# Performance work log

Hardware: AMD Instinct MI355X
Metric: run time of the kernel (lower is better)

Reference implementation:

```python
import jax, jax.numpy as jnp
import numpy as np

N = 8192   # instances in bag
L = 384    # feature dim (dino_bloom_small -> self.L = 384)
D = 128    # attention hidden dim (self.D)
C = 5      # class_count


def setup_inputs() -> dict:
    key = jax.random.key(0)
    ks = jax.random.split(key, 9)
    s = 0.05
    return {
        "x": jax.random.normal(ks[0], (N, L), dtype=jnp.float32),
        # attention_multi_column: Linear(L,D) -> Tanh -> Linear(D,C)
        "aW1": jax.random.normal(ks[1], (L, D), dtype=jnp.float32) * s,
        "ab1": jax.random.normal(ks[2], (D,), dtype=jnp.float32) * s,
        "aW2": jax.random.normal(ks[3], (D, C), dtype=jnp.float32) * s,
        "ab2": jax.random.normal(ks[4], (C,), dtype=jnp.float32) * s,
        # per-class classifiers: Linear(L,64) -> ReLU -> Linear(64,1), batched over C
        "cW1": jax.random.normal(ks[5], (C, L, 64), dtype=jnp.float32) * s,
        "cb1": jax.random.normal(ks[6], (C, 64), dtype=jnp.float32) * s,
        "cW2": jax.random.normal(ks[7], (C, 64), dtype=jnp.float32) * s,
        "cb2": jax.random.normal(ks[8], (C,), dtype=jnp.float32) * s,
    }


def _pairwise_euclidean(ft):
    # ||a-b|| via Gram expansion; avoids the O(N^2*L) broadcast intermediate
    sq = jnp.sum(ft * ft, axis=1)                      # [N]
    d2 = sq[:, None] + sq[None, :] - 2.0 * (ft @ ft.T)  # [N,N]
    d2 = jnp.maximum(d2, 0.0)
    # safe sqrt (zero on diagonal, matches torch.norm subgradient convention)
    return jnp.where(d2 > 0.0, jnp.sqrt(jnp.where(d2 > 0.0, d2, 1.0)), 0.0)


def reference(x, aW1, ab1, aW2, ab2, cW1, cb1, cW2, cb2):
    ft = x  # encoder is identity for dino_bloom_small
    dist = _pairwise_euclidean(ft)                      # [N,N]
    # multicolumn attention: logits per class, softmax over instances
    att = jnp.tanh(ft @ aW1 + ab1) @ aW2 + ab2          # [N,C]
    att_sm = jax.nn.softmax(att, axis=0)                # softmax over N per class
    bag = att_sm.T @ ft                                 # [C,L] bag features per class
    # per-class classifier heads, batched over class dim
    h = jax.nn.relu(jnp.einsum('cl,clh->ch', bag, cW1) + cb1)  # [C,64]
    pred = jnp.sum(h * cW2, axis=1) + cb2               # [C]
    return pred[None, :], dist
```

## Files before the change

kernel.cpp:

```cpp
#include <hip/hip_runtime.h>
#include <cstdint>
#include <cstddef>

#define N_INST 8192
#define L_DIM  384
#define D_DIM  128
#define C_CLS  5

typedef __bf16 bf16x8 __attribute__((ext_vector_type(8)));
typedef float  f32x4  __attribute__((ext_vector_type(4)));
typedef float  f32x4u __attribute__((ext_vector_type(4), aligned(4)));

typedef __attribute__((address_space(1))) void gvoid_t;
typedef __attribute__((address_space(3))) void lvoid_t;

__device__ __forceinline__ unsigned short f2bf(float f) {
  unsigned u = __float_as_uint(f);
  unsigned r = (u + 0x7FFFu + ((u >> 16) & 1u)) >> 16;
  return (unsigned short)r;
}
__device__ __forceinline__ float bf2f(unsigned short b) {
  return __uint_as_float(((unsigned)b) << 16);
}

__device__ __forceinline__ void gload_lds16(const void* g, void* lds) {
  __builtin_amdgcn_global_load_lds(
      (gvoid_t*)(uintptr_t)g,
      (lvoid_t*)(uint32_t)(uintptr_t)lds,
      16, 0, 0);
}

__global__ __launch_bounds__(256) void prep_x_kernel(
    const float* __restrict__ x, unsigned short* __restrict__ xbf,
    float* __restrict__ sq) {
  int w = threadIdx.x >> 6, lane = threadIdx.x & 63;
  int row = blockIdx.x * 4 + w;
  const float* xr = x + (size_t)row * L_DIM;
  unsigned short* br = xbf + (size_t)row * L_DIM;
  float s = 0.f;
#pragma unroll
  for (int k = 0; k < 6; ++k) {
    float v = xr[lane + 64 * k];
    unsigned short b = f2bf(v);
    br[lane + 64 * k] = b;
    float vb = bf2f(b);
    s = fmaf(vb, vb, s);
  }
#pragma unroll
  for (int off = 32; off; off >>= 1) s += __shfl_down(s, off, 64);
  if (lane == 0) sq[row] = s;
}

__global__ __launch_bounds__(256) void prep_w_kernel(
    const float* __restrict__ aW1, unsigned short* __restrict__ w1t) {
  int idx = blockIdx.x * 256 + threadIdx.x;
  int d = idx / L_DIM, l = idx - d * L_DIM;
  w1t[idx] = f2bf(aW1[(size_t)l * D_DIM + d]);
}

__global__ __launch_bounds__(256, 2) void attn_gemm_kernel(
    const unsigned short* __restrict__ amat,
    const unsigned short* __restrict__ bmat,
    const float* __restrict__ bias,
    float* __restrict__ out) {
  __shared__ alignas(16) unsigned short As[128][64];
  __shared__ alignas(16) unsigned short Bs[128][64];

  int tid = threadIdx.x;
  int w = tid >> 6, lane = tid & 63;
  int wr = w >> 1, wc = w & 1;
  int i0 = blockIdx.x * 128;

  const unsigned short* asrc = amat + (size_t)i0 * L_DIM;
  const unsigned short* bsrc = bmat;

  f32x4 acc[4][4];
#pragma unroll
  for (int m = 0; m < 4; ++m)
#pragma unroll
    for (int n = 0; n < 4; ++n) acc[m][n] = (f32x4){0.f, 0.f, 0.f, 0.f};

  int lrow = lane & 15, lkb = lane >> 4;

  for (int kc = 0; kc < 6; ++kc) {
    int k0 = kc * 64;
#pragma unroll
    for (int c = 0; c < 4; ++c) {
      int rb = c * 32 + w * 8;
      gload_lds16(asrc + (size_t)(rb + (lane >> 3)) * L_DIM + k0 + (lane & 7) * 8,
                  &As[rb][0]);
      gload_lds16(bsrc + (size_t)(rb + (lane >> 3)) * L_DIM + k0 + (lane & 7) * 8,
                  &Bs[rb][0]);
    }
    __syncthreads();
#pragma unroll
    for (int kk = 0; kk < 64; kk += 32) {
      bf16x8 af[4], bfr[4];
#pragma unroll
      for (int m = 0; m < 4; ++m)
        af[m] = *(const bf16x8*)&As[wr * 64 + m * 16 + lrow][kk + lkb * 8];
#pragma unroll
      for (int n = 0; n < 4; ++n)
        bfr[n] = *(const bf16x8*)&Bs[wc * 64 + n * 16 + lrow][kk + lkb * 8];
#pragma unroll
      for (int m = 0; m < 4; ++m)
#pragma unroll
        for (int n = 0; n < 4; ++n)
          acc[m][n] = __builtin_amdgcn_mfma_f32_16x16x32_bf16(
              bfr[n], af[m], acc[m][n], 0, 0, 0);
    }
    __syncthreads();
  }
#pragma unroll
  for (int m = 0; m < 4; ++m) {
    int gi = i0 + wr * 64 + m * 16 + lrow;
    float* orow = out + (size_t)gi * D_DIM;
#pragma unroll
    for (int n = 0; n < 4; ++n) {
      int d0 = wc * 64 + n * 16 + lkb * 4;
      f32x4 bv = *(const f32x4*)&bias[d0];
      f32x4 o;
#pragma unroll
      for (int r = 0; r < 4; ++r) o[r] = tanhf(acc[m][n][r] + bv[r]);
      *(f32x4*)&orow[d0] = o;
    }
  }
}

__global__ __launch_bounds__(256, 2) void dist_kernel(
    const unsigned short* __restrict__ xbf, const float* __restrict__ sqv,
    float* __restrict__ F) {
  __shared__ alignas(16) unsigned short As[128][64];
  __shared__ alignas(16) unsigned short Bs[128][64];

  int tid = threadIdx.x;
  int w = tid >> 6, lane = tid & 63;
  int wr = w >> 1, wc = w & 1;

  int b = blockIdx.x;
  int bs = (b & 7) * 512 + (b >> 3);
  int ti = bs >> 6, tj = bs & 63;
  int i0 = ti * 128, j0 = tj * 128;

  const unsigned short* asrc = xbf + (size_t)i0 * L_DIM;
  const unsigned short* bsrc = xbf + (size_t)j0 * L_DIM;

  f32x4 acc[4][4];
#pragma unroll
  for (int m = 0; m < 4; ++m)
#pragma unroll
    for (int n = 0; n < 4; ++n) acc[m][n] = (f32x4){0.f, 0.f, 0.f, 0.f};

  int lrow = lane & 15, lkb = lane >> 4;

  for (int kc = 0; kc < 6; ++kc) {
    int k0 = kc * 64;
#pragma unroll
    for (int c = 0; c < 4; ++c) {
      int rb = c * 32 + w * 8;
      gload_lds16(asrc + (size_t)(rb + (lane >> 3)) * L_DIM + k0 + (lane & 7) * 8,
                  &As[rb][0]);
      gload_lds16(bsrc + (size_t)(rb + (lane >> 3)) * L_DIM + k0 + (lane & 7) * 8,
                  &Bs[rb][0]);
    }
    __syncthreads();
#pragma unroll
    for (int kk = 0; kk < 64; kk += 32) {
      bf16x8 af[4], bfr[4];
#pragma unroll
      for (int m = 0; m < 4; ++m)
        af[m] = *(const bf16x8*)&As[wr * 64 + m * 16 + lrow][kk + lkb * 8];
#pragma unroll
      for (int n = 0; n < 4; ++n)
        bfr[n] = *(const bf16x8*)&Bs[wc * 64 + n * 16 + lrow][kk + lkb * 8];
#pragma unroll
      for (int m = 0; m < 4; ++m)
#pragma unroll
        for (int n = 0; n < 4; ++n)
          acc[m][n] = __builtin_amdgcn_mfma_f32_16x16x32_bf16(
              bfr[n], af[m], acc[m][n], 0, 0, 0);
    }
    __syncthreads();
  }

#pragma unroll
  for (int m = 0; m < 4; ++m) {
    int gi = i0 + wr * 64 + m * 16 + lrow;
    float si = sqv[gi];
    float* orow = F + 5 + (size_t)gi * N_INST;
#pragma unroll
    for (int n = 0; n < 4; ++n) {
      int gjb = j0 + wc * 64 + n * 16 + lkb * 4;
      f32x4 sj = *(const f32x4*)&sqv[gjb];
      f32x4u o;
#pragma unroll
      for (int r = 0; r < 4; ++r) {
        float d2 = si + sj[r] - 2.f * acc[m][n][r];
        float dv = (d2 > 0.f) ? sqrtf(d2) : 0.f;
        if (gi == gjb + r) dv = 0.f;
        o[r] = dv;
      }
      *(f32x4u*)&orow[gjb] = o;
    }
  }
}

__global__ __launch_bounds__(256) void attc_kernel(
    const float* __restrict__ h, const float* __restrict__ aW2,
    const float* __restrict__ ab2, float* __restrict__ exp_att,
    float* __restrict__ colsum) {
  __shared__ float csum[C_CLS];
  if (threadIdx.x < C_CLS) csum[threadIdx.x] = 0.f;
  __syncthreads();
  int i = blockIdx.x * 256 + threadIdx.x;
  float a[C_CLS];
#pragma unroll
  for (int c = 0; c < C_CLS; ++c) a[c] = ab2[c];
  const float* hr = h + (size_t)i * D_DIM;
  for (int d = 0; d < D_DIM; ++d) {
    float hv = hr[d];
#pragma unroll
    for (int c = 0; c < C_CLS; ++c) a[c] = fmaf(hv, aW2[d * C_CLS + c], a[c]);
  }
#pragma unroll
  for (int c = 0; c < C_CLS; ++c) {
    float e = expf(a[c]);
    exp_att[(size_t)i * C_CLS + c] = e;
    atomicAdd(&csum[c], e);
  }
  __syncthreads();
  if (threadIdx.x < C_CLS) atomicAdd(&colsum[threadIdx.x], csum[threadIdx.x]);
}

__global__ __launch_bounds__(256) void bag_kernel(
    const float* __restrict__ x, const float* __restrict__ exp_att,
    float* __restrict__ bagU) {
  int t = threadIdx.x;
  int rbase = blockIdx.x * 32;
  float acc0[C_CLS] = {0, 0, 0, 0, 0}, acc1[C_CLS] = {0, 0, 0, 0, 0};
  int l0 = t, l1 = t + 256;
  for (int i = rbase; i < rbase + 32; ++i) {
    const float* xr = x + (size_t)i * L_DIM;
    float e[C_CLS];
#pragma unroll
    for (int c = 0; c < C_CLS; ++c) e[c] = exp_att[(size_t)i * C_CLS + c];
    float x0 = xr[l0];
#pragma unroll
    for (int c = 0; c < C_CLS; ++c) acc0[c] = fmaf(e[c], x0, acc0[c]);
    if (t < 128) {
      float x1 = xr[l1];
#pragma unroll
      for (int c = 0; c < C_CLS; ++c) acc1[c] = fmaf(e[c], x1, acc1[c]);
    }
  }
#pragma unroll
  for (int c = 0; c < C_CLS; ++c) atomicAdd(&bagU[c * L_DIM + l0], acc0[c]);
  if (t < 128)
#pragma unroll
    for (int c = 0; c < C_CLS; ++c) atomicAdd(&bagU[c * L_DIM + l1], acc1[c]);
}

__global__ __launch_bounds__(256) void final_kernel(
    const float* __restrict__ bagU, const float* __restrict__ colsum,
    const float* __restrict__ cW1, const float* __restrict__ cb1,
    const float* __restrict__ cW2, const float* __restrict__ cb2,
    float* __restrict__ out) {
  __shared__ float bag_s[C_CLS * L_DIM];
  __shared__ float h_s[C_CLS * 64];
  int t = threadIdx.x;
  for (int idx = t; idx < C_CLS * L_DIM; idx += 256) {
    int c = idx / L_DIM;
    bag_s[idx] = bagU[idx] / colsum[c];
  }
  __syncthreads();
  for (int idx = t; idx < C_CLS * 64; idx += 256) {
    int c = idx >> 6, hh = idx & 63;
    float acc = cb1[idx];
    for (int l = 0; l < L_DIM; ++l)
      acc = fmaf(bag_s[c * L_DIM + l], cW1[(size_t)(c * L_DIM + l) * 64 + hh], acc);
    h_s[idx] = fmaxf(acc, 0.f) * cW2[idx];
  }
  __syncthreads();
  if (t < C_CLS) {
    float p = cb2[t];
    for (int hh = 0; hh < 64; ++hh) p += h_s[t * 64 + hh];
    out[t] = p;
  }
}

extern "C" void kernel_launch(void* const* d_in, const int* in_sizes, int n_in,
                              void* d_out, int out_size, void* d_ws,
                              size_t ws_size, hipStream_t stream) {
  const float* x   = (const float*)d_in[0];
  const float* aW1 = (const float*)d_in[1];
  const float* ab1 = (const float*)d_in[2];
  const float* aW2 = (const float*)d_in[3];
  const float* ab2 = (const float*)d_in[4];
  const float* cW1 = (const float*)d_in[5];
  const float* cb1 = (const float*)d_in[6];
  const float* cW2 = (const float*)d_in[7];
  const float* cb2 = (const float*)d_in[8];
  float* outp = (float*)d_out;

  char* ws = (char*)d_ws;
  unsigned short* xbf = (unsigned short*)(ws);
  unsigned short* w1t = (unsigned short*)(ws + 6291456);
  float* sq           = (float*)(ws + 6389760);
  float* h_tanh       = (float*)(ws + 6422528);
  float* exp_att      = (float*)(ws + 10616832);
  float* colsum       = (float*)(ws + 10780672);
  float* bagU         = (float*)(ws + 10780736);

  hipMemsetAsync(ws + 10780672, 0, 64 + C_CLS * L_DIM * 4, stream);

  prep_x_kernel<<<2048, 256, 0, stream>>>(x, xbf, sq);
  prep_w_kernel<<<192, 256, 0, stream>>>(aW1, w1t);
  attn_gemm_kernel<<<64, 256, 0, stream>>>(xbf, w1t, ab1, h_tanh);
  attc_kernel<<<32, 256, 0, stream>>>(h_tanh, aW2, ab2, exp_att, colsum);
  bag_kernel<<<256, 256, 0, stream>>>(x, exp_att, bagU);
  final_kernel<<<1, 256, 0, stream>>>(bagU, colsum, cW1, cb1, cW2, cb2, outp);
  dist_kernel<<<4096, 256, 0, stream>>>(xbf, sq, outp);
}
```

Before: 214.1 us.

## Load dist GEMM operands directly from global, drop LDS staging, loop over column tiles

The distance kernel no longer stages A and B tiles through shared memory with syncthreads. Each wave now reads its bf16 MFMA fragments straight from global memory, relying on L1/L2 caching. Each block now walks four consecutive 128-column tiles, so the grid shrinks from 4096 to 1024 blocks, and launch bounds allow four blocks per CU. This removes LDS traffic and barriers in exchange for uncoalesced 16-byte global loads and duplicate fragment reads across waves.

```diff
diff --git a/kernel.cpp b/kernel.cpp
--- a/kernel.cpp
+++ b/kernel.cpp
@@ -127,52 +127,41 @@
   }
 }
 
-__global__ __launch_bounds__(256, 2) void dist_kernel(
+__global__ __launch_bounds__(256, 4) void dist_kernel(
     const unsigned short* __restrict__ xbf, const float* __restrict__ sqv,
     float* __restrict__ F) {
-  __shared__ alignas(16) unsigned short As[128][64];
-  __shared__ alignas(16) unsigned short Bs[128][64];
-
   int tid = threadIdx.x;
   int w = tid >> 6, lane = tid & 63;
   int wr = w >> 1, wc = w & 1;
+  int lrow = lane & 15, lkb = lane >> 4;
 
   int b = blockIdx.x;
-  int bs = (b & 7) * 512 + (b >> 3);
-  int ti = bs >> 6, tj = bs & 63;
-  int i0 = ti * 128, j0 = tj * 128;
-
-  const unsigned short* asrc = xbf + (size_t)i0 * L_DIM;
-  const unsigned short* bsrc = xbf + (size_t)j0 * L_DIM;
-
-  f32x4 acc[4][4];
-#pragma unroll
-  for (int m = 0; m < 4; ++m)
-#pragma unroll
-    for (int n = 0; n < 4; ++n) acc[m][n] = (f32x4){0.f, 0.f, 0.f, 0.f};
-
-  int lrow = lane & 15, lkb = lane >> 4;
-
-  for (int kc = 0; kc < 6; ++kc) {
-    int k0 = kc * 64;
-#pragma unroll
-    for (int c = 0; c < 4; ++c) {
-      int rb = c * 32 + w * 8;
-      gload_lds16(asrc + (size_t)(rb + (lane >> 3)) * L_DIM + k0 + (lane & 7) * 8,
-                  &As[rb][0]);
-      gload_lds16(bsrc + (size_t)(rb + (lane >> 3)) * L_DIM + k0 + (lane & 7) * 8,
-                  &Bs[rb][0]);
-    }
-    __syncthreads();
-#pragma unroll
-    for (int kk = 0; kk < 64; kk += 32) {
+  int ti = b >> 4, jc = b & 15;
+  int i0 = ti * 128;
+
+  const unsigned short* abase =
+      xbf + (size_t)(i0 + wr * 64 + lrow) * L_DIM + lkb * 8;
+
+#pragma unroll 1
+  for (int js = 0; js < 4; ++js) {
+    int j0 = jc * 512 + js * 128;
+    const unsigned short* bbase =
+        xbf + (size_t)(j0 + wc * 64 + lrow) * L_DIM + lkb * 8;
+
+    f32x4 acc[4][4];
+#pragma unroll
+    for (int m = 0; m < 4; ++m)
+#pragma unroll
+      for (int n = 0; n < 4; ++n) acc[m][n] = (f32x4){0.f, 0.f, 0.f, 0.f};
+
+    for (int t = 0; t < 12; ++t) {
       bf16x8 af[4], bfr[4];
 #pragma unroll
       for (int m = 0; m < 4; ++m)
-        af[m] = *(const bf16x8*)&As[wr * 64 + m * 16 + lrow][kk + lkb * 8];
+        af[m] = *(const bf16x8*)(abase + (size_t)m * 16 * L_DIM + t * 32);
 #pragma unroll
       for (int n = 0; n < 4; ++n)
-        bfr[n] = *(const bf16x8*)&Bs[wc * 64 + n * 16 + lrow][kk + lkb * 8];
+        bfr[n] = *(const bf16x8*)(bbase + (size_t)n * 16 * L_DIM + t * 32);
 #pragma unroll
       for (int m = 0; m < 4; ++m)
 #pragma unroll
@@ -180,27 +169,26 @@
           acc[m][n] = __builtin_amdgcn_mfma_f32_16x16x32_bf16(
               bfr[n], af[m], acc[m][n], 0, 0, 0);
     }
-    __syncthreads();
-  }
-
-#pragma unroll
-  for (int m = 0; m < 4; ++m) {
-    int gi = i0 + wr * 64 + m * 16 + lrow;
-    float si = sqv[gi];
-    float* orow = F + 5 + (size_t)gi * N_INST;
-#pragma unroll
-    for (int n = 0; n < 4; ++n) {
-      int gjb = j0 + wc * 64 + n * 16 + lkb * 4;
-      f32x4 sj = *(const f32x4*)&sqv[gjb];
-      f32x4u o;
-#pragma unroll
-      for (int r = 0; r < 4; ++r) {
-        float d2 = si + sj[r] - 2.f * acc[m][n][r];
-        float dv = (d2 > 0.f) ? sqrtf(d2) : 0.f;
-        if (gi == gjb + r) dv = 0.f;
-        o[r] = dv;
+
+#pragma unroll
+    for (int m = 0; m < 4; ++m) {
+      int gi = i0 + wr * 64 + m * 16 + lrow;
+      float si = sqv[gi];
+      float* orow = F + 5 + (size_t)gi * N_INST;
+#pragma unroll
+      for (int n = 0; n < 4; ++n) {
+        int gjb = j0 + wc * 64 + n * 16 + lkb * 4;
+        f32x4 sj = *(const f32x4*)&sqv[gjb];
+        f32x4u o;
+#pragma unroll
+        for (int r = 0; r < 4; ++r) {
+          float d2 = si + sj[r] - 2.f * acc[m][n][r];
+          float dv = (d2 > 0.f) ? sqrtf(d2) : 0.f;
+          if (gi == gjb + r) dv = 0.f;
+          o[r] = dv;
+        }
+        *(f32x4u*)&orow[gjb] = o;
       }
-      *(f32x4u*)&orow[gjb] = o;
     }
   }
 }
@@ -319,5 +307,5 @@
   attc_kernel<<<32, 256, 0, stream>>>(h_tanh, aW2, ab2, exp_att, colsum);
   bag_kernel<<<256, 256, 0, stream>>>(x, exp_att, bagU);
   final_kernel<<<1, 256, 0, stream>>>(bagU, colsum, cW1, cb1, cW2, cb2, outp);
-  dist_kernel<<<4096, 256, 0, stream>>>(xbf, sq, outp);
-}
+  dist_kernel<<<1024, 256, 0, stream>>>(xbf, sq, outp);
+}
```

Measured after the change: 529.5 us. +147.4%, slower.
